# Performance work log

Measured on AMD Instinct MI355X. Metric: run time of the kernel, lower is better.

## Reference

```python
import jax, jax.numpy as jnp
import numpy as np

N, C_IN, H, W = 32, 128, 56, 56
C_OUT, KH, KW = 256, 3, 3
STRIDE = (1, 1)
PAD = (1, 1)


def setup_inputs() -> dict:
    key = jax.random.key(0)
    k_x, k_w, k_b = jax.random.split(key, 3)
    x = jax.random.normal(k_x, (N, C_IN, H, W), dtype=jnp.float32)
    # kaiming_uniform-like scale for weight, uniform bias in [-1/sqrt(fan_in), 1/sqrt(fan_in)]
    fan_in = C_IN * KH * KW
    bound_w = float(np.sqrt(6.0 / ((1 + 5.0) * fan_in)))  # kaiming_uniform a=sqrt(5)
    weight = jax.random.uniform(k_w, (C_OUT, C_IN, KH, KW), dtype=jnp.float32,
                                minval=-bound_w, maxval=bound_w)
    bound_b = float(1.0 / np.sqrt(fan_in))
    bias = jax.random.uniform(k_b, (C_OUT,), dtype=jnp.float32,
                              minval=-bound_b, maxval=bound_b)
    return {"x": x, "weight": weight, "bias": bias}


def reference(x, weight, bias):
    # Faithful math of the im2col conv: zero padding (ph,pw)=(1,1), stride 1,
    # groups=1 -> identical to a standard cross-correlation conv2d + bias.
    out = jax.lax.conv_general_dilated(
        x, weight,
        window_strides=STRIDE,
        padding=[(PAD[0], PAD[0]), (PAD[1], PAD[1])],
        dimension_numbers=("NCHW", "OIHW", "NCHW"),
    )
    return out + bias[None, :, None, None]
```

## Files before the change

### kernel.cpp

```cpp
#include <hip/hip_runtime.h>


#define NB   32
#define CIN  128
#define HH   56
#define WWD  56
#define COUT 256
#define HWP  3136
#define KTOT 1152
#define HP   58
#define XTN  (HP*HP*CIN)

typedef __bf16 bf16x8 __attribute__((ext_vector_type(8)));
typedef float  f32x4  __attribute__((ext_vector_type(4)));
typedef unsigned short u16;
typedef u16 u16x4 __attribute__((ext_vector_type(4)));
typedef u16 u16x8 __attribute__((ext_vector_type(8)));

__device__ __forceinline__ u16 f2b(float f) {
  unsigned u = __float_as_uint(f);
  u += 0x7fffu + ((u >> 16) & 1u);
  return (u16)(u >> 16);
}

__device__ __forceinline__ void load_lds16(const u16* g, u16* l) {
  __builtin_amdgcn_global_load_lds(
      (const __attribute__((address_space(1))) unsigned int*)g,
      (__attribute__((address_space(3))) unsigned int*)l, 16, 0, 0);
}

__global__ __launch_bounds__(256) void k_transpose_x(const float* __restrict__ x,
                                                     u16* __restrict__ xt) {
  __shared__ u16 tile[64][68];
  const int n  = blockIdx.z;
  const int p0 = blockIdx.x * 64;
  const int c0 = blockIdx.y * 64;
  const int t  = threadIdx.x;

  const float* xp = x + (size_t)n * CIN * HWP + (size_t)c0 * HWP + p0;
  const int pl = (t & 15) * 4;
  const int cr = t >> 4;
#pragma unroll
  for (int j = 0; j < 4; ++j) {
    int c = cr + j * 16;
    f32x4 v = *(const f32x4*)&xp[(size_t)c * HWP + pl];
    u16x4 h;
    h[0] = f2b(v[0]); h[1] = f2b(v[1]); h[2] = f2b(v[2]); h[3] = f2b(v[3]);
    *(u16x4*)&tile[c][pl] = h;
  }
  __syncthreads();
  u16* xb = xt + (size_t)n * XTN + c0;
  const int ch = (t & 7) * 8;
  const int pr = t >> 3;
#pragma unroll
  for (int j = 0; j < 2; ++j) {
    int p  = pr + j * 32;
    int s  = p0 + p;
    int oh = s / WWD;
    int ow = s - oh * WWD;
    u16x8 o;
#pragma unroll
    for (int i = 0; i < 8; ++i) o[i] = tile[ch + i][p];
    *(u16x8*)&xb[((size_t)(oh + 1) * HP + (ow + 1)) * CIN + ch] = o;
  }
}

__global__ __launch_bounds__(256) void k_transform_w(const float* __restrict__ w,
                                                     u16* __restrict__ Wt,
                                                     u16* __restrict__ xt) {
  int o = blockIdx.x * 256 + threadIdx.x;
  if (o < COUT * KTOT) {
    int co  = o / KTOT;
    int rem = o - co * KTOT;
    int kk  = rem >> 7;
    int ci  = rem & 127;
    int kh  = kk / 3;
    int kw  = kk - kh * 3;
    Wt[o] = f2b(w[(((size_t)co * CIN + ci) * 3 + kh) * 3 + kw]);
  }
#pragma unroll
  for (int j = 0; j < 4; ++j) {
    unsigned e = (unsigned)o + j * 294912u;
    if (e < 933888u) {
      unsigned n  = e / 29184u;
      unsigned rm = e - n * 29184u;
      unsigned bp = rm >> 7;
      unsigned ch = rm & 127u;
      unsigned ih, iw;
      if (bp < 58u)       { ih = 0;  iw = bp; }
      else if (bp < 116u) { ih = 57; iw = bp - 58u; }
      else { unsigned c2 = bp - 116u; ih = 1u + (c2 >> 1); iw = (c2 & 1u) ? 57u : 0u; }
      xt[(((size_t)n * HP + ih) * HP + iw) * CIN + ch] = (u16)0;
    }
  }
}


__device__ __forceinline__ int uX_off(int kt) {
  int ksp = kt >> 1;
  int kh  = (ksp >= 6) ? 2 : ((ksp >= 3) ? 1 : 0);
  int kw  = ksp - kh * 3;
  return (kh * HP + kw) * CIN + ((kt & 1) << 6);
}

#define STG(buf_, uxo_, uwo_) do { _Pragma("unroll") \
  for (int c = 0; c < 4; ++c) { \
    load_lds16(Wt + pbW[c] + (uwo_), &lW[buf_][ldo[c]]); \
    load_lds16(xt + pbX[c] + (uxo_), &lX[buf_][ldo[c]]); } } while (0)

#define CMP(buf_) do { _Pragma("unroll") for (int kk = 0; kk < 2; ++kk) { \
    bf16x8 a[4], b[4]; const int sw = ((kk * 4 + q) ^ r7) * 8; \
    _Pragma("unroll") for (int ti = 0; ti < 4; ++ti) \
      a[ti] = *(const bf16x8*)&lX[buf_][(wm + ti * 16 + r) * 64 + sw]; \
    _Pragma("unroll") for (int tj = 0; tj < 4; ++tj) \
      b[tj] = *(const bf16x8*)&lW[buf_][(wc + tj * 16 + r) * 64 + sw]; \
    _Pragma("unroll") for (int ti = 0; ti < 4; ++ti) \
      _Pragma("unroll") for (int tj = 0; tj < 4; ++tj) \
        acc[ti][tj] = __builtin_amdgcn_mfma_f32_16x16x32_bf16( \
            a[ti], b[tj], acc[ti][tj], 0, 0, 0); } } while (0)

__global__ __launch_bounds__(256, 2) void k_conv_gemm(
    const u16* __restrict__ xt, const u16* __restrict__ Wt,
    const float* __restrict__ bias, float* __restrict__ out) {
  __shared__ u16 lW[2][8192];
  __shared__ u16 lX[2][8192];

  const int tid  = threadIdx.x;
  const int wave = tid >> 6;
  const int lane = tid & 63;

  const int bid  = blockIdx.x;
  const int orig = (bid & 7) * 196 + (bid >> 3);
  const int by   = orig / 784;
  const int bx   = orig - by * 784;
  const int m0   = bx * 128;
  const int co0  = by * 128;

  const int r  = lane & 15;
  const int q  = lane >> 4;
  const int r7 = r & 7;
  const int wm = (wave & 1) * 64;
  const int wc = (wave >> 1) * 64;

  const int rsub = lane >> 3;
  const int pso  = ((lane & 7) ^ rsub) * 8;

  int pbX[4], pbW[4], ldo[4];
#pragma unroll
  for (int c = 0; c < 4; ++c) {
    const int rowb = wave * 32 + c * 8;
    const int m  = m0 + rowb + rsub;
    const int n  = m / HWP;
    const int s  = m - n * HWP;
    const int oh = s / WWD;
    const int ow = s - oh * WWD;
    pbX[c] = ((n * HP + oh) * HP + ow) * CIN + pso;
    pbW[c] = (co0 + rowb + rsub) * KTOT + pso;
    ldo[c] = rowb * 64;
  }
  float bias_r[4];
#pragma unroll
  for (int tj = 0; tj < 4; ++tj) bias_r[tj] = bias[co0 + wc + tj * 16 + r];

  f32x4 acc[4][4];
#pragma unroll
  for (int i = 0; i < 4; ++i)
#pragma unroll
    for (int j = 0; j < 4; ++j) acc[i][j] = (f32x4){0.f, 0.f, 0.f, 0.f};

  STG(0, 0, 0);
  asm volatile("s_waitcnt vmcnt(0)" ::: "memory");
  __builtin_amdgcn_s_barrier();

#pragma unroll 1
  for (int p = 0; p < 8; ++p) {
    const int kt = p * 2;
    STG(1, uX_off(kt + 1), (kt + 1) * 64);
    CMP(0);
    asm volatile("s_waitcnt vmcnt(0)" ::: "memory");
    __builtin_amdgcn_s_barrier();
    STG(0, uX_off(kt + 2), (kt + 2) * 64);
    CMP(1);
    asm volatile("s_waitcnt vmcnt(0)" ::: "memory");
    __builtin_amdgcn_s_barrier();
  }
  STG(1, uX_off(17), 17 * 64);
  CMP(0);
  asm volatile("s_waitcnt vmcnt(0)" ::: "memory");
  __builtin_amdgcn_s_barrier();
  CMP(1);

#pragma unroll
  for (int ti = 0; ti < 4; ++ti) {
    const int m4 = m0 + wm + ti * 16 + q * 4;
    const int n  = m4 / HWP;
    const int s  = m4 - n * HWP;
    float* op = out + (size_t)n * COUT * HWP + s;
#pragma unroll
    for (int tj = 0; tj < 4; ++tj) {
      const int co = co0 + wc + tj * 16 + r;
      f32x4 v = acc[ti][tj];
      const float bv = bias_r[tj];
      v[0] += bv; v[1] += bv; v[2] += bv; v[3] += bv;
      *(f32x4*)(op + (size_t)co * HWP) = v;
    }
  }
}

extern "C" void kernel_launch(void* const* d_in, const int* in_sizes, int n_in,
                              void* d_out, int out_size, void* d_ws, size_t ws_size,
                              hipStream_t stream) {
  const float* x    = (const float*)d_in[0];
  const float* w    = (const float*)d_in[1];
  const float* bias = (const float*)d_in[2];
  float* out        = (float*)d_out;

  u16* xt = (u16*)d_ws;
  u16* Wt = xt + (size_t)NB * XTN;

  k_transform_w<<<dim3(1152), dim3(256), 0, stream>>>(w, Wt, xt);
  k_transpose_x<<<dim3(49, 2, 32), dim3(256), 0, stream>>>(x, xt);
  k_conv_gemm<<<dim3(1568), dim3(256), 0, stream>>>(xt, Wt, bias, out);
}
```

Before: 218.8 us.

## Replace LDS double buffering with single buffer and raise occupancy to four blocks

The implicit-GEMM conv loop drops its two-stage LDS ping-pong for a single LDS buffer per operand, with a barrier before and after each K-step load. This halves LDS per block and raises the launch-bounds occupancy hint from 2 to 4 blocks per CU, so latency is hidden by more resident waves instead of software prefetch. Block-index decoding also changes so the two output-channel tiles of the same pixel tile are neighbours, which should improve L2 reuse of the input tile. In exchange, each iteration now stalls on its own global-to-LDS load, and correctness relies on __syncthreads waiting for the LDS-DMA loads, since the explicit vmcnt wait was removed.

Measured after the change: 207.0 us. 1.06x faster.

```diff
diff --git a/kernel.cpp b/kernel.cpp
--- a/kernel.cpp
+++ b/kernel.cpp
@@ -103,27 +103,11 @@
   return (kh * HP + kw) * CIN + ((kt & 1) << 6);
 }
 
-#define STG(buf_, uxo_, uwo_) do { _Pragma("unroll") \
-  for (int c = 0; c < 4; ++c) { \
-    load_lds16(Wt + pbW[c] + (uwo_), &lW[buf_][ldo[c]]); \
-    load_lds16(xt + pbX[c] + (uxo_), &lX[buf_][ldo[c]]); } } while (0)
-
-#define CMP(buf_) do { _Pragma("unroll") for (int kk = 0; kk < 2; ++kk) { \
-    bf16x8 a[4], b[4]; const int sw = ((kk * 4 + q) ^ r7) * 8; \
-    _Pragma("unroll") for (int ti = 0; ti < 4; ++ti) \
-      a[ti] = *(const bf16x8*)&lX[buf_][(wm + ti * 16 + r) * 64 + sw]; \
-    _Pragma("unroll") for (int tj = 0; tj < 4; ++tj) \
-      b[tj] = *(const bf16x8*)&lW[buf_][(wc + tj * 16 + r) * 64 + sw]; \
-    _Pragma("unroll") for (int ti = 0; ti < 4; ++ti) \
-      _Pragma("unroll") for (int tj = 0; tj < 4; ++tj) \
-        acc[ti][tj] = __builtin_amdgcn_mfma_f32_16x16x32_bf16( \
-            a[ti], b[tj], acc[ti][tj], 0, 0, 0); } } while (0)
-
-__global__ __launch_bounds__(256, 2) void k_conv_gemm(
+__global__ __launch_bounds__(256, 4) void k_conv_gemm(
     const u16* __restrict__ xt, const u16* __restrict__ Wt,
     const float* __restrict__ bias, float* __restrict__ out) {
-  __shared__ u16 lW[2][8192];
-  __shared__ u16 lX[2][8192];
+  __shared__ u16 lW[8192];
+  __shared__ u16 lX[8192];
 
   const int tid  = threadIdx.x;
   const int wave = tid >> 6;
@@ -131,8 +115,8 @@
 
   const int bid  = blockIdx.x;
   const int orig = (bid & 7) * 196 + (bid >> 3);
-  const int by   = orig / 784;
-  const int bx   = orig - by * 784;
+  const int bx   = orig >> 1;
+  const int by   = orig & 1;
   const int m0   = bx * 128;
   const int co0  = by * 128;
 
@@ -168,27 +152,36 @@
 #pragma unroll
     for (int j = 0; j < 4; ++j) acc[i][j] = (f32x4){0.f, 0.f, 0.f, 0.f};
 
-  STG(0, 0, 0);
-  asm volatile("s_waitcnt vmcnt(0)" ::: "memory");
-  __builtin_amdgcn_s_barrier();
-
 #pragma unroll 1
-  for (int p = 0; p < 8; ++p) {
-    const int kt = p * 2;
-    STG(1, uX_off(kt + 1), (kt + 1) * 64);
-    CMP(0);
-    asm volatile("s_waitcnt vmcnt(0)" ::: "memory");
-    __builtin_amdgcn_s_barrier();
-    STG(0, uX_off(kt + 2), (kt + 2) * 64);
-    CMP(1);
-    asm volatile("s_waitcnt vmcnt(0)" ::: "memory");
-    __builtin_amdgcn_s_barrier();
-  }
-  STG(1, uX_off(17), 17 * 64);
-  CMP(0);
-  asm volatile("s_waitcnt vmcnt(0)" ::: "memory");
-  __builtin_amdgcn_s_barrier();
-  CMP(1);
+  for (int kt = 0; kt < 18; ++kt) {
+    const int uxo = uX_off(kt);
+    const int uwo = kt * 64;
+    __syncthreads();
+#pragma unroll
+    for (int c = 0; c < 4; ++c) {
+      load_lds16(xt + pbX[c] + uxo, &lX[ldo[c]]);
+      load_lds16(Wt + pbW[c] + uwo, &lW[ldo[c]]);
+    }
+    __syncthreads();
+
+#pragma unroll
+    for (int kk = 0; kk < 2; ++kk) {
+      bf16x8 a[4], b[4];
+      const int sw = ((kk * 4 + q) ^ r7) * 8;
+#pragma unroll
+      for (int ti = 0; ti < 4; ++ti)
+        a[ti] = *(const bf16x8*)&lX[(wm + ti * 16 + r) * 64 + sw];
+#pragma unroll
+      for (int tj = 0; tj < 4; ++tj)
+        b[tj] = *(const bf16x8*)&lW[(wc + tj * 16 + r) * 64 + sw];
+#pragma unroll
+      for (int ti = 0; ti < 4; ++ti)
+#pragma unroll
+        for (int tj = 0; tj < 4; ++tj)
+          acc[ti][tj] = __builtin_amdgcn_mfma_f32_16x16x32_bf16(
+              a[ti], b[tj], acc[ti][tj], 0, 0, 0);
+    }
+  }
 
 #pragma unroll
   for (int ti = 0; ti < 4; ++ti) {
```
